# Optimization experiments

Hardware: AMD Instinct MI355X
Metric: run time of the kernel (lower is better)

Reference implementation:

```python
import jax, jax.numpy as jnp
import numpy as np

B, T, C, F = 2, 2048, 2048, 8192
LN_EPS = 1e-5


def setup_inputs() -> dict:
    key = jax.random.key(0)
    ks = jax.random.split(key, 24)
    rn = lambda k, s, sc=1.0: jax.random.normal(k, s, jnp.float32) * sc
    un = lambda k, s: jax.random.uniform(k, s, jnp.float32)
    inp = {}
    inp['x'] = rn(ks[0], (B, T, C))
    inp['att_shift'] = rn(ks[1], (B, C))
    # wkv_state rows: aa (num), bb (den), pp (running max exponent)
    inp['wkv_state'] = jnp.stack([jnp.zeros((B, C)), jnp.zeros((B, C)),
                                  jnp.full((B, C), -1e38)], axis=1)
    inp['ffn_shift'] = rn(ks[2], (B, C))
    inp['ln1_g'] = jnp.ones(C); inp['ln1_b'] = jnp.zeros(C)
    inp['ln2_g'] = jnp.ones(C); inp['ln2_b'] = jnp.zeros(C)
    inp['tmk'] = un(ks[3], (C,)); inp['tmv'] = un(ks[4], (C,)); inp['tmr'] = un(ks[5], (C,))
    inp['time_decay'] = rn(ks[6], (C,), 0.5)
    inp['time_first'] = rn(ks[7], (C,), 0.5)
    inp['Wk'] = rn(ks[8], (C, C), 0.02); inp['Wv'] = rn(ks[9], (C, C), 0.02)
    inp['Wr'] = rn(ks[10], (C, C), 0.02); inp['Wo'] = rn(ks[11], (C, C), 0.02)
    inp['fmk'] = un(ks[12], (C,)); inp['fmr'] = un(ks[13], (C,))
    inp['Fk'] = rn(ks[14], (C, F), 0.02)
    inp['Fr'] = rn(ks[15], (C, C), 0.02)
    inp['Fv'] = rn(ks[16], (F, C), 0.02)
    return inp


def layer_norm(x, g, b):
    m = jnp.mean(x, axis=-1, keepdims=True)
    v = jnp.mean(jnp.square(x - m), axis=-1, keepdims=True)
    return (x - m) * jax.lax.rsqrt(v + LN_EPS) * g + b


def wkv(w, u, k, v, state):
    # w: -exp(time_decay) [C], u: time_first [C]; k,v: [B,T,C]; state: [B,3,C]
    def step(carry, kv_t):
        aa, bb, pp = carry
        kt, vt = kv_t
        ww = u + kt
        p = jnp.maximum(pp, ww)
        e1 = jnp.exp(pp - p)
        e2 = jnp.exp(ww - p)
        y = (e1 * aa + e2 * vt) / (e1 * bb + e2)
        ww2 = pp + w
        p2 = jnp.maximum(ww2, kt)
        e1b = jnp.exp(ww2 - p2)
        e2b = jnp.exp(kt - p2)
        return (e1b * aa + e2b * vt, e1b * bb + e2b, p2), y
    carry0 = (state[:, 0], state[:, 1], state[:, 2])
    (aa, bb, pp), ys = jax.lax.scan(step, carry0,
                                    (k.transpose(1, 0, 2), v.transpose(1, 0, 2)))
    return ys.transpose(1, 0, 2), jnp.stack([aa, bb, pp], axis=1)


def reference(x, att_shift, wkv_state, ffn_shift, ln1_g, ln1_b, ln2_g, ln2_b,
              tmk, tmv, tmr, time_decay, time_first, Wk, Wv, Wr, Wo,
              fmk, fmr, Fk, Fr, Fv):
    # ---- time-mix (attention) ----
    x1 = layer_norm(x, ln1_g, ln1_b)
    xx = jnp.concatenate([att_shift[:, None, :], x1[:, :-1]], axis=1)
    xk = x1 * tmk + xx * (1.0 - tmk)
    xv = x1 * tmv + xx * (1.0 - tmv)
    xr = x1 * tmr + xx * (1.0 - tmr)
    k = jnp.einsum('btc,cd->btd', xk, Wk)
    v = jnp.einsum('btc,cd->btd', xv, Wv)
    r = jnp.einsum('btc,cd->btd', xr, Wr)
    y, new_wkv = wkv(-jnp.exp(time_decay), time_first, k, v, wkv_state)
    x = x + jnp.einsum('btd,dc->btc', jax.nn.sigmoid(r) * y, Wo)
    # ---- channel-mix (FFN) ----
    x2 = layer_norm(x, ln2_g, ln2_b)
    xx2 = jnp.concatenate([ffn_shift[:, None, :], x2[:, :-1]], axis=1)
    xk2 = x2 * fmk + xx2 * (1.0 - fmk)
    xr2 = x2 * fmr + xx2 * (1.0 - fmr)
    kf = jnp.square(jax.nn.relu(jnp.einsum('btc,cf->btf', xk2, Fk)))
    kv = jnp.einsum('btf,fc->btc', kf, Fv)
    x = x + jax.nn.sigmoid(jnp.einsum('btc,cd->btd', xr2, Fr)) * kv
    return x, x1[:, -1], new_wkv, x2[:, -1]
```

## Files before the change

kernel.cpp:

```cpp
#include <hip/hip_runtime.h>
#include <stdint.h>

#define B_ 2
#define T_ 2048
#define C_ 2048
#define F_ 8192
#define M_ 4096
#define BC_ 4096
#define CHB 16
#define TCH 16
#define LC2 128

typedef __attribute__((ext_vector_type(8))) __bf16 bf16x8;
typedef __attribute__((ext_vector_type(4))) float f32x4;

__device__ __forceinline__ unsigned short f2bf(float f) {
  union { float f; unsigned u; } v; v.f = f;
  unsigned r = v.u + 0x7fffu + ((v.u >> 16) & 1u);
  return (unsigned short)(r >> 16);
}
__device__ __forceinline__ float b2f(unsigned short h) {
  union { unsigned u; float f; } v; v.u = ((unsigned)h) << 16; return v.f;
}

__device__ __forceinline__ void gload16(const void* g, void* l) {
  __builtin_amdgcn_global_load_lds((__attribute__((address_space(1))) void*)g,
                                   (__attribute__((address_space(3))) void*)l,
                                   16, 0, 0);
}

__device__ __forceinline__ void transpose_tile(
    const float* __restrict__ W, unsigned short* __restrict__ out,
    int K, int N, int k0, int n0) {
  __shared__ unsigned short tile[32][66];
  const int tx = threadIdx.x & 31, ty = threadIdx.x >> 5;
#pragma unroll
  for (int i = 0; i < 8; ++i)
    tile[tx][ty + 8 * i] = f2bf(W[(size_t)(k0 + ty + 8 * i) * N + n0 + tx]);
  __syncthreads();
#pragma unroll
  for (int j = 0; j < 4; ++j) {
    const int nn = ty + 8 * j;
    const unsigned pk = *(const unsigned*)&tile[nn][2 * tx];
    *(unsigned*)&out[(size_t)(n0 + nn) * K + k0 + 2 * tx] = pk;
  }
}

__global__ __launch_bounds__(256) void k_transpose4(
    const float* __restrict__ W0, const float* __restrict__ W1,
    const float* __restrict__ W2, const float* __restrict__ W3,
    unsigned short* __restrict__ WT) {
  const float* W = (blockIdx.z == 0) ? W0 : (blockIdx.z == 1) ? W1
                   : (blockIdx.z == 2) ? W2 : W3;
  unsigned short* out = WT + (size_t)blockIdx.z * C_ * C_;
  transpose_tile(W, out, C_, C_, blockIdx.x * 64, blockIdx.y * 32);
}

__global__ __launch_bounds__(256) void k_transpose1(
    const float* __restrict__ W, unsigned short* __restrict__ WT, int K, int N) {
  transpose_tile(W, WT, K, N, blockIdx.x * 64, blockIdx.y * 32);
}

__global__ __launch_bounds__(256) void k_layernorm(
    const float* __restrict__ x, const float* __restrict__ g,
    const float* __restrict__ beta, unsigned short* __restrict__ y,
    float* __restrict__ last_out) {
  const int row = blockIdx.x;
  const int t = row & (T_ - 1);
  const int bi = row >> 11;
  const float* xr = x + (size_t)row * C_;
  const int base = threadIdx.x * 8;
  float lv[8];
  {
    float4 a = *(const float4*)(xr + base);
    float4 b = *(const float4*)(xr + base + 4);
    lv[0]=a.x; lv[1]=a.y; lv[2]=a.z; lv[3]=a.w; lv[4]=b.x; lv[5]=b.y; lv[6]=b.z; lv[7]=b.w;
  }
  float s = 0.f, q = 0.f;
#pragma unroll
  for (int j = 0; j < 8; ++j) { s += lv[j]; q += lv[j] * lv[j]; }
#pragma unroll
  for (int o = 32; o > 0; o >>= 1) { s += __shfl_down(s, o); q += __shfl_down(q, o); }
  __shared__ float rs[4], rq[4];
  if ((threadIdx.x & 63) == 0) { rs[threadIdx.x >> 6] = s; rq[threadIdx.x >> 6] = q; }
  __syncthreads();
  s = rs[0] + rs[1] + rs[2] + rs[3];
  q = rq[0] + rq[1] + rq[2] + rq[3];
  const float mean = s * (1.f / C_);
  const float var = q * (1.f / C_) - mean * mean;
  const float inv = 1.f / sqrtf(var + 1e-5f);
  float ov[8];
  unsigned short o8[8];
#pragma unroll
  for (int j = 0; j < 8; ++j) {
    ov[j] = (lv[j] - mean) * inv * g[base + j] + beta[base + j];
    o8[j] = f2bf(ov[j]);
  }
  *(uint4*)(y + (size_t)row * C_ + base) = *(uint4*)o8;
  if (last_out != nullptr && t == T_ - 1) {
    float* lp = last_out + (size_t)bi * C_ + base;
    *(float4*)lp = make_float4(ov[0], ov[1], ov[2], ov[3]);
    *(float4*)(lp + 4) = make_float4(ov[4], ov[5], ov[6], ov[7]);
  }
}

__global__ __launch_bounds__(256) void k_mix3(
    const unsigned short* __restrict__ x1, const float* __restrict__ shift,
    const float* __restrict__ tmk, const float* __restrict__ tmv,
    const float* __restrict__ tmr,
    unsigned short* __restrict__ xk, unsigned short* __restrict__ xv,
    unsigned short* __restrict__ xr) {
  const int row = blockIdx.x;
  const int t = row & (T_ - 1);
  const int bi = row >> 11;
  const int c0 = threadIdx.x * 8;
  const size_t o = (size_t)row * C_ + c0;
  unsigned short cur8[8];
  *(uint4*)cur8 = *(const uint4*)(x1 + o);
  float pv[8];
  if (t == 0) {
    const float* sp = shift + (size_t)bi * C_ + c0;
#pragma unroll
    for (int j = 0; j < 8; ++j) pv[j] = sp[j];
  } else {
    unsigned short p8[8];
    *(uint4*)p8 = *(const uint4*)(x1 + o - C_);
#pragma unroll
    for (int j = 0; j < 8; ++j) pv[j] = b2f(p8[j]);
  }
  unsigned short ok[8], ov[8], orr[8];
#pragma unroll
  for (int j = 0; j < 8; ++j) {
    const float a = b2f(cur8[j]), p = pv[j];
    const float mk = tmk[c0 + j], mv = tmv[c0 + j], mr = tmr[c0 + j];
    ok[j]  = f2bf(a * mk + p * (1.f - mk));
    ov[j]  = f2bf(a * mv + p * (1.f - mv));
    orr[j] = f2bf(a * mr + p * (1.f - mr));
  }
  *(uint4*)(xk + o) = *(uint4*)ok;
  *(uint4*)(xv + o) = *(uint4*)ov;
  *(uint4*)(xr + o) = *(uint4*)orr;
}

__global__ __launch_bounds__(256) void k_mix2(
    const unsigned short* __restrict__ x2, const float* __restrict__ shift,
    const float* __restrict__ fmk, const float* __restrict__ fmr,
    unsigned short* __restrict__ xk2, unsigned short* __restrict__ xr2) {
  const int row = blockIdx.x;
  const int t = row & (T_ - 1);
  const int bi = row >> 11;
  const int c0 = threadIdx.x * 8;
  const size_t o = (size_t)row * C_ + c0;
  unsigned short cur8[8];
  *(uint4*)cur8 = *(const uint4*)(x2 + o);
  float pv[8];
  if (t == 0) {
    const float* sp = shift + (size_t)bi * C_ + c0;
#pragma unroll
    for (int j = 0; j < 8; ++j) pv[j] = sp[j];
  } else {
    unsigned short p8[8];
    *(uint4*)p8 = *(const uint4*)(x2 + o - C_);
#pragma unroll
    for (int j = 0; j < 8; ++j) pv[j] = b2f(p8[j]);
  }
  unsigned short ok[8], orr[8];
#pragma unroll
  for (int j = 0; j < 8; ++j) {
    const float a = b2f(cur8[j]), p = pv[j];
    const float mk = fmk[c0 + j], mr = fmr[c0 + j];
    ok[j]  = f2bf(a * mk + p * (1.f - mk));
    orr[j] = f2bf(a * mr + p * (1.f - mr));
  }
  *(uint4*)(xk2 + o) = *(uint4*)ok;
  *(uint4*)(xr2 + o) = *(uint4*)orr;
}

__global__ __launch_bounds__(256) void k_wkv_sry(
    const float* __restrict__ kk, const float* __restrict__ vv,
    const unsigned short* __restrict__ rr,
    const float* __restrict__ td, const float* __restrict__ tf,
    const float* __restrict__ st, unsigned short* __restrict__ sry,
    float* __restrict__ out_state) {
  __shared__ float sA[TCH][CHB], sB[TCH][CHB], sP[TCH][CHB];
  const int blk = blockIdx.x;
  const int bi = blk >> 7;
  const int tx = threadIdx.x & 15;
  const int ty = threadIdx.x >> 4;
  const int c = ((blk & 127) * CHB) + tx;
  const float w = -expf(td[c]);
  const float u = tf[c];
  const size_t base = (size_t)bi * T_ * C_ + (size_t)ty * LC2 * C_ + c;
  const float* kp = kk + base;
  const float* vp = vv + base;
  float aa = 0.f, bb = 0.f, pp = -1e38f;
#pragma unroll 8
  for (int i = 0; i < LC2; ++i) {
    const float kt = kp[(size_t)i * C_], vt = vp[(size_t)i * C_];
    const float ww2 = pp + w;
    const float p2 = fmaxf(ww2, kt);
    const float e1b = expf(ww2 - p2), e2b = expf(kt - p2);
    aa = e1b * aa + e2b * vt;
    bb = e1b * bb + e2b;
    pp = p2;
  }
  sA[ty][tx] = aa; sB[ty][tx] = bb; sP[ty][tx] = pp;
  __syncthreads();
  if (ty == 0) {
    const float* s0 = st + (size_t)bi * 3 * C_;
    float ca = s0[c], cb = s0[C_ + c], cp = s0[2 * C_ + c];
    const float wL = w * (float)LC2;
#pragma unroll
    for (int j = 0; j < TCH; ++j) {
      const float a2 = sA[j][tx], b2 = sB[j][tx], p2 = sP[j][tx];
      sA[j][tx] = ca; sB[j][tx] = cb; sP[j][tx] = cp;
      const float pd = cp + wL;
      const float pm = fmaxf(pd, p2);
      const float e1 = expf(pd - pm), e2 = expf(p2 - pm);
      ca = e1 * ca + e2 * a2;
      cb = e1 * cb + e2 * b2;
      cp = pm;
    }
  }
  __syncthreads();
  aa = sA[ty][tx]; bb = sB[ty][tx]; pp = sP[ty][tx];
  const unsigned short* rp = rr + base;
  unsigned short* sp2 = sry + base;
#pragma unroll 4
  for (int i = 0; i < LC2; ++i) {
    const float kt = kp[(size_t)i * C_], vt = vp[(size_t)i * C_];
    const float ww = u + kt;
    const float p = fmaxf(pp, ww);
    const float e1 = expf(pp - p), e2 = expf(ww - p);
    const float yv = (e1 * aa + e2 * vt) / (e1 * bb + e2);
    const float rv = b2f(rp[(size_t)i * C_]);
    const float sg = 1.f / (1.f + expf(-rv));
    sp2[(size_t)i * C_] = f2bf(sg * yv);
    const float ww2 = pp + w;
    const float p2 = fmaxf(ww2, kt);
    const float e1b = expf(ww2 - p2), e2b = expf(kt - p2);
    aa = e1b * aa + e2b * vt;
    bb = e1b * bb + e2b;
    pp = p2;
  }
  if (ty == TCH - 1) {
    float* ob = out_state + (size_t)bi * 3 * C_;
    ob[c] = aa; ob[C_ + c] = bb; ob[2 * C_ + c] = pp;
  }
}

template <int EPI, int SWZ>
__global__ __launch_bounds__(512, 1) void k_gemm8(
    const unsigned short* __restrict__ A, const unsigned short* __restrict__ BT,
    int K, int Nn, void* __restrict__ out,
    const float* __restrict__ aux1, const void* __restrict__ aux2,
    const void* __restrict__ aux3) {
  __shared__ unsigned short lds[73728];
  const int tid = threadIdx.x;
  const int lane = tid & 63;
  const int wid = tid >> 6;
  int mBase, nBase;
  if (SWZ) {
    const int gx = gridDim.x, gy = gridDim.y;
    const int wg = blockIdx.y * gx + blockIdx.x;
    const int per = (gx * gy) >> 3;
    const int p = 31 - __clz(per);
    const int nr = 1 << ((p - 1) >> 1);
    const int mr = per / nr;
    if ((gx % nr) == 0 && (gy % mr) == 0) {
      const int gxr = gx / nr;
      const int xcd = wg & 7, idx = wg >> 3;
      const int rr = xcd / gxr, rc = xcd % gxr;
      mBase = (rr * mr + idx / nr) * 128;
      nBase = (rc * nr + idx % nr) * 256;
    } else {
      int w2 = (wg & 7) * per + (wg >> 3);
      mBase = (w2 / gx) * 128;
      nBase = (w2 % gx) * 256;
    }
  } else {
    mBase = blockIdx.y * 128;
    nBase = blockIdx.x * 256;
  }
  const int wr = (wid >> 2) * 64;
  const int wc = (wid & 3) * 64;
  const int r16 = lane & 15, kq = lane >> 4;
  const int lrow = lane >> 3;
  const int lslot = (lane & 7) ^ lrow;
  const int xsw = r16 & 7;
  f32x4 acc[4][4] = {};

  const unsigned short* gA0 = A  + (size_t)(mBase + 0   + wid * 8 + lrow) * K + lslot * 8;
  const unsigned short* gA1 = A  + (size_t)(mBase + 64  + wid * 8 + lrow) * K + lslot * 8;
  const unsigned short* gB0 = BT + (size_t)(nBase + 0   + wid * 8 + lrow) * K + lslot * 8;
  const unsigned short* gB1 = BT + (size_t)(nBase + 64  + wid * 8 + lrow) * K + lslot * 8;
  const unsigned short* gB2 = BT + (size_t)(nBase + 128 + wid * 8 + lrow) * K + lslot * 8;
  const unsigned short* gB3 = BT + (size_t)(nBase + 192 + wid * 8 + lrow) * K + lslot * 8;
  const int wof = wid * 512;
  int aoff[4][2], boff[4][2];
#pragma unroll
  for (int m = 0; m < 4; ++m)
#pragma unroll
    for (int s = 0; s < 2; ++s)
      aoff[m][s] = (wr + m * 16 + r16) * 64 + (((s * 4 + kq) ^ xsw) * 8);
#pragma unroll
  for (int n = 0; n < 4; ++n)
#pragma unroll
    for (int s = 0; s < 2; ++s)
      boff[n][s] = 8192 + (wc + n * 16 + r16) * 64 + (((s * 4 + kq) ^ xsw) * 8);

  const int nt = K >> 6;
  gload16(gA0, &lds[0 + wof]);
  gload16(gA1, &lds[4096 + wof]);
  gload16(gB0, &lds[8192 + wof]);
  gload16(gB1, &lds[12288 + wof]);
  gload16(gB2, &lds[16384 + wof]);
  gload16(gB3, &lds[20480 + wof]);
  gload16(gA0 + 64, &lds[24576 + 0 + wof]);
  gload16(gA1 + 64, &lds[24576 + 4096 + wof]);
  gload16(gB0 + 64, &lds[24576 + 8192 + wof]);
  gload16(gB1 + 64, &lds[24576 + 12288 + wof]);
  gload16(gB2 + 64, &lds[24576 + 16384 + wof]);
  gload16(gB3 + 64, &lds[24576 + 20480 + wof]);
  asm volatile("s_waitcnt vmcnt(6)" ::: "memory");
  asm volatile("s_barrier" ::: "memory");

  int cb = 0;
  for (int t = 0; t < nt; ++t) {
    const int nb = (cb >= 1) ? cb - 1 : 2;
    const int ca = cb * 24576;
    const int nba = nb * 24576;
    const int kb2 = (t + 2) << 6;
    const bool pf = (t + 2) < nt;
    if (pf) {
      gload16(gA0 + kb2, &lds[nba + 0 + wof]);
      gload16(gA1 + kb2, &lds[nba + 4096 + wof]);
      gload16(gB0 + kb2, &lds[nba + 8192 + wof]);
      gload16(gB1 + kb2, &lds[nba + 12288 + wof]);
      gload16(gB2 + kb2, &lds[nba + 16384 + wof]);
      gload16(gB3 + kb2, &lds[nba + 20480 + wof]);
    }
    bf16x8 af[4][2], bq[4][2];
#pragma unroll
    for (int m = 0; m < 4; ++m)
#pragma unroll
      for (int s = 0; s < 2; ++s)
        af[m][s] = *(const bf16x8*)&lds[ca + aoff[m][s]];
#pragma unroll
    for (int n = 0; n < 4; ++n)
#pragma unroll
      for (int s = 0; s < 2; ++s)
        bq[n][s] = *(const bf16x8*)&lds[ca + boff[n][s]];
    __builtin_amdgcn_s_setprio(1);
#pragma unroll
    for (int m = 0; m < 4; ++m)
#pragma unroll
      for (int n = 0; n < 4; ++n)
#pragma unroll
        for (int s = 0; s < 2; ++s)
          acc[m][n] = __builtin_amdgcn_mfma_f32_16x16x32_bf16(
              af[m][s], bq[n][s], acc[m][n], 0, 0, 0);
    __builtin_amdgcn_s_setprio(0);
    if (pf) {
      asm volatile("s_waitcnt vmcnt(6)" ::: "memory");
    } else if (t + 1 < nt) {
      asm volatile("s_waitcnt vmcnt(0)" ::: "memory");
    }
    asm volatile("s_barrier" ::: "memory");
    cb = (cb == 2) ? 0 : cb + 1;
  }

  const int c0 = kq * 4;
#pragma unroll
  for (int m = 0; m < 4; ++m) {
#pragma unroll
    for (int n = 0; n < 4; ++n) {
      const int col = nBase + wc + n * 16 + r16;
#pragma unroll
      for (int e = 0; e < 4; ++e) {
        const int rowg = mBase + wr + m * 16 + c0 + e;
        const size_t idx = (size_t)rowg * Nn + col;
        const float va = acc[m][n][e];
        if (EPI == 0) {
          ((float*)out)[idx] = va;
        } else if (EPI == 1) {
          const float t = va > 0.f ? va : 0.f;
          ((unsigned short*)out)[idx] = f2bf(t * t);
        } else if (EPI == 2) {
          ((float*)out)[idx] = aux1[idx] + va;
        } else if (EPI == 3) {
          const float s = 1.f / (1.f + expf(-va));
          ((float*)out)[idx] = aux1[idx] + s * ((const float*)aux2)[idx];
        } else if (EPI == 5) {
          const float s = 1.f / (1.f + expf(-va));
          const float kvv = b2f(((const unsigned short*)aux2)[idx]) +
                            b2f(((const unsigned short*)aux3)[idx]);
          ((float*)out)[idx] = aux1[idx] + s * kvv;
        } else {
          ((unsigned short*)out)[idx] = f2bf(va);
        }
      }
    }
  }
}

template <int EPI, int SWZ>
__global__ __launch_bounds__(512, 1) void k_gemm256(
    const unsigned short* __restrict__ A, const unsigned short* __restrict__ BT,
    int K, int Klen, int Nn, void* __restrict__ out, size_t outStride) {
  __shared__ unsigned short lds[65536];
  const int tid = threadIdx.x;
  const int lane = tid & 63;
  const int wid = tid >> 6;
  const int Koff = blockIdx.z * Klen;
  void* outz = (char*)out + (size_t)blockIdx.z * outStride;
  int mBase, nBase;
  if (SWZ) {
    const int gx = gridDim.x, gy = gridDim.y;
    const int wg = blockIdx.y * gx + blockIdx.x;
    const int per = (gx * gy) >> 3;
    const int p = 31 - __clz(per);
    const int nr = 1 << (p >> 1);
    const int mr = per / nr;
    if ((gx % nr) == 0 && (gy % mr) == 0) {
      const int gxr = gx / nr;
      const int xcd = wg & 7, idx = wg >> 3;
      const int rr = xcd / gxr, rc = xcd % gxr;
      mBase = (rr * mr + idx / nr) * 256;
      nBase = (rc * nr + idx % nr) * 256;
    } else {
      int w2 = (wg & 7) * per + (wg >> 3);
      mBase = (w2 / gx) * 256;
      nBase = (w2 % gx) * 256;
    }
  } else {
    mBase = blockIdx.y * 256;
    nBase = blockIdx.x * 256;
  }
  const int wr = (wid >> 2) * 128;
  const int wc = (wid & 3) * 64;
  const int r16 = lane & 15, kq = lane >> 4;
  const int lrow = lane >> 3;
  const int lslot = (lane & 7) ^ lrow;
  const int xsw = r16 & 7;
  f32x4 acc[8][4] = {};

  const unsigned short* gA[4];
  const unsigned short* gB[4];
#pragma unroll
  for (int j = 0; j < 4; ++j) {
    gA[j] = A  + (size_t)(mBase + j * 64 + wid * 8 + lrow) * K + Koff + lslot * 8;
    gB[j] = BT + (size_t)(nBase + j * 64 + wid * 8 + lrow) * K + Koff + lslot * 8;
  }
  const int wof = wid * 512;

  const int nt = Klen >> 6;
#pragma unroll
  for (int j = 0; j < 4; ++j) {
    gload16(gA[j], &lds[j * 4096 + wof]);
    gload16(gB[j], &lds[16384 + j * 4096 + wof]);
  }
  asm volatile("s_waitcnt vmcnt(0)" ::: "memory");
  asm volatile("s_barrier" ::: "memory");

  for (int t = 0; t < nt; ++t) {
    const int ca = (t & 1) * 32768;
    const int nba = ((t + 1) & 1) * 32768;
    const int kb1 = (t + 1) << 6;
    const bool pf = (t + 1) < nt;
    if (pf) {
#pragma unroll
      for (int j = 0; j < 4; ++j) {
        gload16(gA[j] + kb1, &lds[nba + j * 4096 + wof]);
        gload16(gB[j] + kb1, &lds[nba + 16384 + j * 4096 + wof]);
      }
    }
    bf16x8 bq[4][2];
#pragma unroll
    for (int n = 0; n < 4; ++n)
#pragma unroll
      for (int s = 0; s < 2; ++s)
        bq[n][s] = *(const bf16x8*)&lds[ca + 16384 + (wc + n * 16 + r16) * 64 +
                                        (((s * 4 + kq) ^ xsw) * 8)];
#pragma unroll
    for (int qm = 0; qm < 2; ++qm) {
      bf16x8 af[4][2];
#pragma unroll
      for (int m = 0; m < 4; ++m)
#pragma unroll
        for (int s = 0; s < 2; ++s)
          af[m][s] = *(const bf16x8*)&lds[ca + (wr + (qm * 4 + m) * 16 + r16) * 64 +
                                          (((s * 4 + kq) ^ xsw) * 8)];
      __builtin_amdgcn_s_setprio(1);
#pragma unroll
      for (int m = 0; m < 4; ++m)
#pragma unroll
        for (int n = 0; n < 4; ++n)
#pragma unroll
          for (int s = 0; s < 2; ++s)
            acc[qm * 4 + m][n] = __builtin_amdgcn_mfma_f32_16x16x32_bf16(
                af[m][s], bq[n][s], acc[qm * 4 + m][n], 0, 0, 0);
      __builtin_amdgcn_s_setprio(0);
    }
    if (pf) asm volatile("s_waitcnt vmcnt(0)" ::: "memory");
    asm volatile("s_barrier" ::: "memory");
  }

  const int c0 = kq * 4;
#pragma unroll
  for (int m = 0; m < 8; ++m) {
#pragma unroll
    for (int n = 0; n < 4; ++n) {
      const int col = nBase + wc + n * 16 + r16;
#pragma unroll
      for (int e = 0; e < 4; ++e) {
        const int rowg = mBase + wr + m * 16 + c0 + e;
        const size_t idx = (size_t)rowg * Nn + col;
        const float va = acc[m][n][e];
        if (EPI == 0) {
          ((float*)outz)[idx] = va;
        } else if (EPI == 1) {
          const float t = va > 0.f ? va : 0.f;
          ((unsigned short*)outz)[idx] = f2bf(t * t);
        } else {
          ((unsigned short*)outz)[idx] = f2bf(va);
        }
      }
    }
  }
}

extern "C" void kernel_launch(void* const* d_in, const int* in_sizes, int n_in,
                              void* d_out, int out_size, void* d_ws, size_t ws_size,
                              hipStream_t stream) {
  const float* x          = (const float*)d_in[0];
  const float* att_shift  = (const float*)d_in[1];
  const float* wkv_state  = (const float*)d_in[2];
  const float* ffn_shift  = (const float*)d_in[3];
  const float* ln1_g = (const float*)d_in[4];
  const float* ln1_b = (const float*)d_in[5];
  const float* ln2_g = (const float*)d_in[6];
  const float* ln2_b = (const float*)d_in[7];
  const float* tmk = (const float*)d_in[8];
  const float* tmv = (const float*)d_in[9];
  const float* tmr = (const float*)d_in[10];
  const float* time_decay = (const float*)d_in[11];
  const float* time_first = (const float*)d_in[12];
  const float* Wk = (const float*)d_in[13];
  const float* Wv = (const float*)d_in[14];
  const float* Wr = (const float*)d_in[15];
  const float* Wo = (const float*)d_in[16];
  const float* fmk = (const float*)d_in[17];
  const float* fmr = (const float*)d_in[18];
  const float* Fk = (const float*)d_in[19];
  const float* Fr = (const float*)d_in[20];
  const float* Fv = (const float*)d_in[21];

  const size_t MB = 1ull << 20;
  char* ws = (char*)d_ws;
  if (ws_size < 176 * MB) return;

  unsigned short* Wslot = (unsigned short*)(ws);
  float*          kBuf  = (float*)(ws + 32 * MB);
  float*          vBuf  = (float*)(ws + 64 * MB);
  float*          yBuf  = (float*)(ws + 96 * MB);
  unsigned short* h1    = (unsigned short*)(ws + 128 * MB);
  unsigned short* h2    = (unsigned short*)(ws + 144 * MB);
  unsigned short* h3    = (unsigned short*)(ws + 160 * MB);
  unsigned short* xrT   = (unsigned short*)kBuf;
  unsigned short* kf    = (unsigned short*)kBuf;
  unsigned short* kvp   = (unsigned short*)h1;
  unsigned short* sWr = Wslot + 0 * (size_t)C_ * C_;
  unsigned short* sWk = Wslot + 1 * (size_t)C_ * C_;
  unsigned short* sWv = Wslot + 2 * (size_t)C_ * C_;
  unsigned short* sWo = Wslot + 3 * (size_t)C_ * C_;

  float* outb    = (float*)d_out;
  float* x1_last = outb + (size_t)M_ * C_;
  float* wkv_out = x1_last + (size_t)B_ * C_;
  float* x2_last = wkv_out + (size_t)B_ * 3 * C_;

  const dim3 gC8(C_ / 256, M_ / 128);
  const dim3 gF256(F_ / 256, M_ / 256);
  const dim3 gKV(C_ / 256, M_ / 256, 2);

  k_transpose4<<<dim3(C_ / 64, C_ / 32, 4), 256, 0, stream>>>(Wr, Wk, Wv, Wo, Wslot);
  k_layernorm<<<M_, 256, 0, stream>>>(x, ln1_g, ln1_b, h1, x1_last);
  k_mix3<<<M_, 256, 0, stream>>>(h1, att_shift, tmk, tmv, tmr, h2, h3, xrT);
  k_gemm8<4,1><<<gC8, 512, 0, stream>>>(xrT, sWr, C_, C_, h1, nullptr, nullptr, nullptr);
  k_gemm8<0,1><<<gC8, 512, 0, stream>>>(h2, sWk, C_, C_, kBuf, nullptr, nullptr, nullptr);
  k_gemm8<0,1><<<gC8, 512, 0, stream>>>(h3, sWv, C_, C_, vBuf, nullptr, nullptr, nullptr);
  k_wkv_sry<<<dim3(BC_ / CHB), 256, 0, stream>>>(kBuf, vBuf, h1, time_decay, time_first,
                                                 wkv_state, h2, wkv_out);
  k_gemm8<2,1><<<gC8, 512, 0, stream>>>(h2, sWo, C_, C_, yBuf, x, nullptr, nullptr);

  k_layernorm<<<M_, 256, 0, stream>>>(yBuf, ln2_g, ln2_b, h1, x2_last);
  k_mix2<<<M_, 256, 0, stream>>>(h1, ffn_shift, fmk, fmr, h2, h3);
  k_transpose1<<<dim3(C_ / 64, F_ / 32), 256, 0, stream>>>(Fk, Wslot, C_, F_);
  k_gemm256<1,1><<<gF256, 512, 0, stream>>>(h2, Wslot, C_, C_, F_, kf, 0);
  k_transpose1<<<dim3(F_ / 64, C_ / 32), 256, 0, stream>>>(Fv, Wslot, F_, C_);
  k_gemm256<4,1><<<gKV, 512, 0, stream>>>(kf, Wslot, F_, F_ / 2, C_, kvp, 16 * MB);
  k_transpose1<<<dim3(C_ / 64, C_ / 32), 256, 0, stream>>>(Fr, Wslot, C_, C_);
  k_gemm8<5,1><<<gC8, 512, 0, stream>>>(h3, Wslot, C_, C_, d_out, yBuf,
                                        kvp, kvp + 8 * (size_t)MB);
}
```

Baseline: 618.0 us.

## Fuse K, V, R projection GEMMs into one batched 256x256-tile launch

New measurement: 629.3 us. Within noise of the previous version (+1.8%).

```diff
diff --git a/kernel.cpp b/kernel.cpp
--- a/kernel.cpp
+++ b/kernel.cpp
@@ -404,47 +404,18 @@
   }
 }
 
-template <int EPI, int SWZ>
-__global__ __launch_bounds__(512, 1) void k_gemm256(
+__device__ __forceinline__ void gemm256_core(
     const unsigned short* __restrict__ A, const unsigned short* __restrict__ BT,
-    int K, int Klen, int Nn, void* __restrict__ out, size_t outStride) {
-  __shared__ unsigned short lds[65536];
-  const int tid = threadIdx.x;
-  const int lane = tid & 63;
-  const int wid = tid >> 6;
-  const int Koff = blockIdx.z * Klen;
-  void* outz = (char*)out + (size_t)blockIdx.z * outStride;
-  int mBase, nBase;
-  if (SWZ) {
-    const int gx = gridDim.x, gy = gridDim.y;
-    const int wg = blockIdx.y * gx + blockIdx.x;
-    const int per = (gx * gy) >> 3;
-    const int p = 31 - __clz(per);
-    const int nr = 1 << (p >> 1);
-    const int mr = per / nr;
-    if ((gx % nr) == 0 && (gy % mr) == 0) {
-      const int gxr = gx / nr;
-      const int xcd = wg & 7, idx = wg >> 3;
-      const int rr = xcd / gxr, rc = xcd % gxr;
-      mBase = (rr * mr + idx / nr) * 256;
-      nBase = (rc * nr + idx % nr) * 256;
-    } else {
-      int w2 = (wg & 7) * per + (wg >> 3);
-      mBase = (w2 / gx) * 256;
-      nBase = (w2 % gx) * 256;
-    }
-  } else {
-    mBase = blockIdx.y * 256;
-    nBase = blockIdx.x * 256;
-  }
+    int K, int Klen, int Koff, int mBase, int nBase,
+    unsigned short* lds, f32x4 (&acc)[8][4]) {
+  const int lane = threadIdx.x & 63;
+  const int wid = threadIdx.x >> 6;
   const int wr = (wid >> 2) * 128;
   const int wc = (wid & 3) * 64;
   const int r16 = lane & 15, kq = lane >> 4;
   const int lrow = lane >> 3;
   const int lslot = (lane & 7) ^ lrow;
   const int xsw = r16 & 7;
-  f32x4 acc[8][4] = {};
-
   const unsigned short* gA[4];
   const unsigned short* gB[4];
 #pragma unroll
@@ -453,7 +424,6 @@
     gB[j] = BT + (size_t)(nBase + j * 64 + wid * 8 + lrow) * K + Koff + lslot * 8;
   }
   const int wof = wid * 512;
-
   const int nt = Klen >> 6;
 #pragma unroll
   for (int j = 0; j < 4; ++j) {
@@ -505,7 +475,41 @@
     if (pf) asm volatile("s_waitcnt vmcnt(0)" ::: "memory");
     asm volatile("s_barrier" ::: "memory");
   }
-
+}
+
+__device__ __forceinline__ void swz256(int gx, int gy, int& mBase, int& nBase) {
+  const int wg = blockIdx.y * gx + blockIdx.x;
+  const int per = (gx * gy) >> 3;
+  const int p = 31 - __clz(per);
+  const int nr = 1 << (p >> 1);
+  const int mr = per / nr;
+  if ((gx % nr) == 0 && (gy % mr) == 0) {
+    const int gxr = gx / nr;
+    const int xcd = wg & 7, idx = wg >> 3;
+    const int rr = xcd / gxr, rc = xcd % gxr;
+    mBase = (rr * mr + idx / nr) * 256;
+    nBase = (rc * nr + idx % nr) * 256;
+  } else {
+    int w2 = (wg & 7) * per + (wg >> 3);
+    mBase = (w2 / gx) * 256;
+    nBase = (w2 % gx) * 256;
+  }
+}
+
+template <int EPI>
+__global__ __launch_bounds__(512, 1) void k_gemm256(
+    const unsigned short* __restrict__ A, const unsigned short* __restrict__ BT,
+    int K, int Klen, int Nn, void* __restrict__ out, size_t outStride) {
+  __shared__ unsigned short lds[65536];
+  int mBase, nBase;
+  swz256(gridDim.x, gridDim.y, mBase, nBase);
+  void* outz = (char*)out + (size_t)blockIdx.z * outStride;
+  f32x4 acc[8][4] = {};
+  gemm256_core(A, BT, K, Klen, blockIdx.z * Klen, mBase, nBase, lds, acc);
+  const int lane = threadIdx.x & 63;
+  const int wid = threadIdx.x >> 6;
+  const int wr = (wid >> 2) * 128, wc = (wid & 3) * 64;
+  const int r16 = lane & 15, kq = lane >> 4;
   const int c0 = kq * 4;
 #pragma unroll
   for (int m = 0; m < 8; ++m) {
@@ -517,14 +521,50 @@
         const int rowg = mBase + wr + m * 16 + c0 + e;
         const size_t idx = (size_t)rowg * Nn + col;
         const float va = acc[m][n][e];
-        if (EPI == 0) {
-          ((float*)outz)[idx] = va;
-        } else if (EPI == 1) {
+        if (EPI == 1) {
           const float t = va > 0.f ? va : 0.f;
           ((unsigned short*)outz)[idx] = f2bf(t * t);
         } else {
           ((unsigned short*)outz)[idx] = f2bf(va);
         }
+      }
+    }
+  }
+}
+
+__global__ __launch_bounds__(512, 1) void k_gemm_kvr(
+    const unsigned short* __restrict__ xk, const unsigned short* __restrict__ xv,
+    const unsigned short* __restrict__ xr,
+    const unsigned short* __restrict__ sWk, const unsigned short* __restrict__ sWv,
+    const unsigned short* __restrict__ sWr,
+    float* __restrict__ kOut, float* __restrict__ vOut,
+    unsigned short* __restrict__ rOut) {
+  __shared__ unsigned short lds[65536];
+  const int z = blockIdx.z;
+  const unsigned short* A  = (z == 0) ? xk  : (z == 1) ? xv  : xr;
+  const unsigned short* BT = (z == 0) ? sWk : (z == 1) ? sWv : sWr;
+  int mBase, nBase;
+  swz256(gridDim.x, gridDim.y, mBase, nBase);
+  f32x4 acc[8][4] = {};
+  gemm256_core(A, BT, C_, C_, 0, mBase, nBase, lds, acc);
+  const int lane = threadIdx.x & 63;
+  const int wid = threadIdx.x >> 6;
+  const int wr = (wid >> 2) * 128, wc = (wid & 3) * 64;
+  const int r16 = lane & 15, kq = lane >> 4;
+  const int c0 = kq * 4;
+#pragma unroll
+  for (int m = 0; m < 8; ++m) {
+#pragma unroll
+    for (int n = 0; n < 4; ++n) {
+      const int col = nBase + wc + n * 16 + r16;
+#pragma unroll
+      for (int e = 0; e < 4; ++e) {
+        const int rowg = mBase + wr + m * 16 + c0 + e;
+        const size_t idx = (size_t)rowg * C_ + col;
+        const float va = acc[m][n][e];
+        if (z == 0)      kOut[idx] = va;
+        else if (z == 1) vOut[idx] = va;
+        else             rOut[idx] = f2bf(va);
       }
     }
   }
@@ -567,7 +607,7 @@
   unsigned short* h1    = (unsigned short*)(ws + 128 * MB);
   unsigned short* h2    = (unsigned short*)(ws + 144 * MB);
   unsigned short* h3    = (unsigned short*)(ws + 160 * MB);
-  unsigned short* xrT   = (unsigned short*)kBuf;
+  unsigned short* xrB   = (unsigned short*)yBuf;
   unsigned short* kf    = (unsigned short*)kBuf;
   unsigned short* kvp   = (unsigned short*)h1;
   unsigned short* sWr = Wslot + 0 * (size_t)C_ * C_;
@@ -583,13 +623,13 @@
   const dim3 gC8(C_ / 256, M_ / 128);
   const dim3 gF256(F_ / 256, M_ / 256);
   const dim3 gKV(C_ / 256, M_ / 256, 2);
+  const dim3 gKVR(C_ / 256, M_ / 256, 3);
 
   k_transpose4<<<dim3(C_ / 64, C_ / 32, 4), 256, 0, stream>>>(Wr, Wk, Wv, Wo, Wslot);
   k_layernorm<<<M_, 256, 0, stream>>>(x, ln1_g, ln1_b, h1, x1_last);
-  k_mix3<<<M_, 256, 0, stream>>>(h1, att_shift, tmk, tmv, tmr, h2, h3, xrT);
-  k_gemm8<4,1><<<gC8, 512, 0, stream>>>(xrT, sWr, C_, C_, h1, nullptr, nullptr, nullptr);
-  k_gemm8<0,1><<<gC8, 512, 0, stream>>>(h2, sWk, C_, C_, kBuf, nullptr, nullptr, nullptr);
-  k_gemm8<0,1><<<gC8, 512, 0, stream>>>(h3, sWv, C_, C_, vBuf, nullptr, nullptr, nullptr);
+  k_mix3<<<M_, 256, 0, stream>>>(h1, att_shift, tmk, tmv, tmr, h2, h3, xrB);
+  k_gemm_kvr<<<gKVR, 512, 0, stream>>>(h2, h3, xrB, sWk, sWv, sWr,
+                                       kBuf, vBuf, h1);
   k_wkv_sry<<<dim3(BC_ / CHB), 256, 0, stream>>>(kBuf, vBuf, h1, time_decay, time_first,
                                                  wkv_state, h2, wkv_out);
   k_gemm8<2,1><<<gC8, 512, 0, stream>>>(h2, sWo, C_, C_, yBuf, x, nullptr, nullptr);
@@ -597,9 +637,9 @@
   k_layernorm<<<M_, 256, 0, stream>>>(yBuf, ln2_g, ln2_b, h1, x2_last);
   k_mix2<<<M_, 256, 0, stream>>>(h1, ffn_shift, fmk, fmr, h2, h3);
   k_transpose1<<<dim3(C_ / 64, F_ / 32), 256, 0, stream>>>(Fk, Wslot, C_, F_);
-  k_gemm256<1,1><<<gF256, 512, 0, stream>>>(h2, Wslot, C_, C_, F_, kf, 0);
+  k_gemm256<1><<<gF256, 512, 0, stream>>>(h2, Wslot, C_, C_, F_, kf, 0);
   k_transpose1<<<dim3(F_ / 64, C_ / 32), 256, 0, stream>>>(Fv, Wslot, F_, C_);
-  k_gemm256<4,1><<<gKV, 512, 0, stream>>>(kf, Wslot, F_, F_ / 2, C_, kvp, 16 * MB);
+  k_gemm256<4><<<gKV, 512, 0, stream>>>(kf, Wslot, F_, F_ / 2, C_, kvp, 16 * MB);
   k_transpose1<<<dim3(C_ / 64, C_ / 32), 256, 0, stream>>>(Fr, Wslot, C_, C_);
   k_gemm8<5,1><<<gC8, 512, 0, stream>>>(h3, Wslot, C_, C_, d_out, yBuf,
                                         kvp, kvp + 8 * (size_t)MB);
```
